# Performance work log

Hardware: AMD Instinct MI355X
Metric: run time of the kernel (lower is better)

Reference implementation:

```python
import jax, jax.numpy as jnp
import numpy as np


def setup_inputs() -> dict:
    key = jax.random.key(0)
    ks = jax.random.split(key, 8)
    B, C, H, W = 32, 98, 128, 128
    F, D = 256, 128
    return {
        "hm": jax.random.normal(ks[0], (B, C, H, W), dtype=jnp.float32),
        "feat": jax.random.normal(ks[1], (B, F, H, W), dtype=jnp.float32),
        "W_embed": jax.random.normal(ks[2], (2 + 1 + F, D), dtype=jnp.float32) * 0.05,
        "b_embed": jax.random.normal(ks[3], (D,), dtype=jnp.float32) * 0.05,
        "A": jax.random.normal(ks[4], (C, C), dtype=jnp.float32) * 0.05,
        "W_gcn": jax.random.normal(ks[5], (D, D), dtype=jnp.float32) * 0.05,
        "W_out": jax.random.normal(ks[6], (D, 2), dtype=jnp.float32) * 0.05,
        "b_out": jax.random.normal(ks[7], (2,), dtype=jnp.float32) * 0.05,
    }


def reference(hm, feat, W_embed, b_embed, A, W_gcn, W_out, b_out):
    # hm: [B, C, H, W] per-landmark heatmaps; feat: [B, F, H, W] backbone features.
    B, C, H, W = hm.shape
    F = feat.shape[1]

    # decode_heatmap: per-(batch, landmark) argmax location over HxW (batched,
    # replacing the original per-sample Python loops).
    hm_flat = hm.reshape(B, C, H * W)
    idx = jnp.argmax(hm_flat, axis=-1)                      # [B, C] int
    ys = idx // W
    xs = idx % W

    # node confidences: hm[i, classIds, ys, xs] -> batched gather
    conf = jnp.take_along_axis(hm_flat, idx[:, :, None], axis=-1)[..., 0]  # [B, C]

    # pooling_feature: gather the F-dim feature vector at each landmark location
    feat_flat = feat.reshape(B, F, H * W)
    vis = jnp.take_along_axis(feat_flat, idx[:, None, :], axis=-1)  # [B, F, C]
    vis = jnp.transpose(vis, (0, 2, 1))                              # [B, C, F]

    # normalized positions: node_positions (x, y) / hm_size [h, w] (as in source)
    hm_size = jnp.array([H, W], dtype=hm.dtype)
    pos = jnp.stack([xs, ys], axis=-1).astype(hm.dtype) / hm_size    # [B, C, 2]

    # GCN over landmarks (batched instead of per-sample calls)
    node = jnp.concatenate([pos, conf[..., None], vis], axis=-1)     # [B, C, 2+1+F]
    h0 = jax.nn.relu(jnp.einsum("bcf,fd->bcd", node, W_embed) + b_embed)
    h1 = jax.nn.relu(jnp.einsum("ij,bjd,de->bie", A, h0, W_gcn))     # learned adjacency
    out = jnp.einsum("bcd,do->bco", h1, W_out) + b_out               # [B, C, 2]
    return hm, out
```

## Files before the change

kernel.cpp:

```cpp
#include <hip/hip_runtime.h>

#define HM_B 32
#define HM_C 98
#define HM_H 128
#define HM_W 128
#define HWSZ (HM_H * HM_W)
#define FDIM 256
#define DDIM 128
#define NODE_F (2 + 1 + FDIM)
#define NODE_P 260
#define BC (HM_B * HM_C)
#define HM_ELEMS ((size_t)BC * HWSZ)
#define LCHUNK 8
#define ICHUNK 7
#define NTHR 256
#define NWAVE (NTHR / 64)

typedef float f32x4 __attribute__((ext_vector_type(4)));

__global__ __launch_bounds__(NTHR) void k1_copy_argmax(
    const float* __restrict__ hm, float* __restrict__ out_hm,
    float* __restrict__ pconf, int* __restrict__ pidx) {
    const int row = blockIdx.x;
    const int tid = threadIdx.x;
    const f32x4* __restrict__ src = (const f32x4*)(hm + (size_t)row * HWSZ);
    f32x4* __restrict__ dst = (f32x4*)(out_hm + (size_t)row * HWSZ);

    float bv = -INFINITY;
    int bi = 0;
    f32x4 cur0 = src[0 * NTHR + tid];
    f32x4 cur1 = src[1 * NTHR + tid];
    f32x4 cur2 = src[2 * NTHR + tid];
    f32x4 cur3 = src[3 * NTHR + tid];
    #pragma unroll
    for (int g = 0; g < 4; ++g) {
        f32x4 nxt0, nxt1, nxt2, nxt3;
        if (g < 3) {
            nxt0 = src[((g + 1) * 4 + 0) * NTHR + tid];
            nxt1 = src[((g + 1) * 4 + 1) * NTHR + tid];
            nxt2 = src[((g + 1) * 4 + 2) * NTHR + tid];
            nxt3 = src[((g + 1) * 4 + 3) * NTHR + tid];
        }
        #pragma unroll
        for (int u = 0; u < 4; ++u) {
            const f32x4 v = (u == 0) ? cur0 : (u == 1) ? cur1 : (u == 2) ? cur2 : cur3;
            const int p = (g * 4 + u) * NTHR + tid;
            __builtin_nontemporal_store(v, dst + p);
            const float m4 = fmaxf(fmaxf(v[0], v[1]), fmaxf(v[2], v[3]));
            if (m4 > bv) {
                const int base = p * 4;
                if (v[0] > bv) { bv = v[0]; bi = base; }
                if (v[1] > bv) { bv = v[1]; bi = base + 1; }
                if (v[2] > bv) { bv = v[2]; bi = base + 2; }
                if (v[3] > bv) { bv = v[3]; bi = base + 3; }
            }
        }
        cur0 = nxt0; cur1 = nxt1; cur2 = nxt2; cur3 = nxt3;
    }

    #pragma unroll
    for (int s = 1; s < 64; s <<= 1) {
        const float ov = __shfl_xor(bv, s, 64);
        const int oi = __shfl_xor(bi, s, 64);
        if (ov > bv || (ov == bv && oi < bi)) { bv = ov; bi = oi; }
    }
    if ((tid & 63) == 0) {
        pconf[row * NWAVE + (tid >> 6)] = bv;
        pidx[row * NWAVE + (tid >> 6)] = bi;
    }
}

__global__ __launch_bounds__(NTHR) void k2_embed(
    const float* __restrict__ feat, const float* __restrict__ pconf,
    const int* __restrict__ pidx, const float* __restrict__ W_embed,
    const float* __restrict__ b_embed, float* __restrict__ h0_ws) {
    const int bc0 = blockIdx.x * LCHUNK;
    const int tid = threadIdx.x;
    __shared__ float node_s[LCHUNK][NODE_P];
    __shared__ int locs[LCHUNK];

    if (tid < LCHUNK) {
        const int row = bc0 + tid;
        float fv = pconf[row * NWAVE];
        int fi = pidx[row * NWAVE];
        #pragma unroll
        for (int w = 1; w < NWAVE; ++w) {
            const float ov = pconf[row * NWAVE + w];
            const int oi = pidx[row * NWAVE + w];
            if (ov > fv || (ov == fv && oi < fi)) { fv = ov; fi = oi; }
        }
        locs[tid] = fi;
        node_s[tid][0] = (float)(fi % HM_W) * (1.0f / (float)HM_H);
        node_s[tid][1] = (float)(fi / HM_W) * (1.0f / (float)HM_W);
        node_s[tid][2] = fv;
    }
    __syncthreads();

    float g[LCHUNK];
    #pragma unroll
    for (int l = 0; l < LCHUNK; ++l) {
        const int bb = (bc0 + l) / HM_C;
        g[l] = __builtin_nontemporal_load(
            feat + ((size_t)(bb * FDIM + tid)) * HWSZ + locs[l]);
    }
    #pragma unroll
    for (int l = 0; l < LCHUNK; ++l)
        node_s[l][3 + tid] = g[l];
    __syncthreads();

    const int d = tid & (DDIM - 1);
    const int lbase = (tid >> 7) * 4;
    const float bias = b_embed[d];
    float a0 = bias, a1 = bias, a2 = bias, a3 = bias;
    for (int f = 0; f < NODE_F; ++f) {
        const float w = W_embed[f * DDIM + d];
        a0 = fmaf(node_s[lbase + 0][f], w, a0);
        a1 = fmaf(node_s[lbase + 1][f], w, a1);
        a2 = fmaf(node_s[lbase + 2][f], w, a2);
        a3 = fmaf(node_s[lbase + 3][f], w, a3);
    }
    h0_ws[(size_t)(bc0 + lbase + 0) * DDIM + d] = fmaxf(a0, 0.f);
    h0_ws[(size_t)(bc0 + lbase + 1) * DDIM + d] = fmaxf(a1, 0.f);
    h0_ws[(size_t)(bc0 + lbase + 2) * DDIM + d] = fmaxf(a2, 0.f);
    h0_ws[(size_t)(bc0 + lbase + 3) * DDIM + d] = fmaxf(a3, 0.f);
}

__global__ __launch_bounds__(DDIM) void k3_gcn(
    const float* __restrict__ A, const float* __restrict__ h0_ws,
    const float* __restrict__ W_gcn, const float* __restrict__ W_out,
    const float* __restrict__ b_out, float* __restrict__ out2) {
    const int b = blockIdx.x / (HM_C / ICHUNK);
    const int i0 = (blockIdx.x % (HM_C / ICHUNK)) * ICHUNK;
    const int tid = threadIdx.x;

    __shared__ float arow[ICHUNK * HM_C];
    __shared__ float tmp_s[ICHUNK * DDIM];
    __shared__ float h1_s[ICHUNK * DDIM];

    for (int k = tid; k < ICHUNK * HM_C; k += DDIM)
        arow[k] = A[(i0 + k / HM_C) * HM_C + (k % HM_C)];
    __syncthreads();

    {
        float acc[ICHUNK];
        #pragma unroll
        for (int i = 0; i < ICHUNK; ++i) acc[i] = 0.f;
        for (int j = 0; j < HM_C; ++j) {
            const float v = h0_ws[((size_t)b * HM_C + j) * DDIM + tid];
            #pragma unroll
            for (int i = 0; i < ICHUNK; ++i)
                acc[i] = fmaf(arow[i * HM_C + j], v, acc[i]);
        }
        #pragma unroll
        for (int i = 0; i < ICHUNK; ++i) tmp_s[i * DDIM + tid] = acc[i];
    }
    __syncthreads();

    {
        float acc[ICHUNK];
        #pragma unroll
        for (int i = 0; i < ICHUNK; ++i) acc[i] = 0.f;
        for (int k = 0; k < DDIM; ++k) {
            const float w = W_gcn[k * DDIM + tid];
            #pragma unroll
            for (int i = 0; i < ICHUNK; ++i)
                acc[i] = fmaf(tmp_s[i * DDIM + k], w, acc[i]);
        }
        #pragma unroll
        for (int i = 0; i < ICHUNK; ++i) h1_s[i * DDIM + tid] = fmaxf(acc[i], 0.f);
    }
    __syncthreads();

    if (tid < ICHUNK * 2) {
        const int i = tid >> 1;
        const int o = tid & 1;
        float acc = b_out[o];
        for (int dd = 0; dd < DDIM; ++dd)
            acc = fmaf(h1_s[i * DDIM + dd], W_out[dd * 2 + o], acc);
        out2[((size_t)b * HM_C + i0 + i) * 2 + o] = acc;
    }
}

extern "C" void kernel_launch(void* const* d_in, const int* in_sizes, int n_in,
                              void* d_out, int out_size, void* d_ws, size_t ws_size,
                              hipStream_t stream) {
    const float* hm      = (const float*)d_in[0];
    const float* feat    = (const float*)d_in[1];
    const float* W_embed = (const float*)d_in[2];
    const float* b_embed = (const float*)d_in[3];
    const float* A       = (const float*)d_in[4];
    const float* W_gcn   = (const float*)d_in[5];
    const float* W_out   = (const float*)d_in[6];
    const float* b_out   = (const float*)d_in[7];

    float* out_hm = (float*)d_out;
    float* out2   = (float*)d_out + HM_ELEMS;

    char* ws = (char*)d_ws;
    float* pconf = (float*)ws;  ws += BC * NWAVE * sizeof(float);
    int*   pidx  = (int*)ws;    ws += BC * NWAVE * sizeof(int);
    float* h0_ws = (float*)ws;

    k1_copy_argmax<<<BC, NTHR, 0, stream>>>(hm, out_hm, pconf, pidx);
    k2_embed<<<BC / LCHUNK, NTHR, 0, stream>>>(feat, pconf, pidx,
                                               W_embed, b_embed, h0_ws);
    k3_gcn<<<HM_B * (HM_C / ICHUNK), DDIM, 0, stream>>>(A, h0_ws, W_gcn,
                                                        W_out, b_out, out2);
}
```

Before: 109.6 us.

## Split fused heatmap copy and argmax into separate kernels

Separates the heatmap passthrough copy from the per-row argmax reduction. The argmax kernel now loads all 16 vectors per thread up front, and a grid-stride kernel with a fixed block count does the nontemporal copy. This decouples the store traffic from the reduction, but the heatmap is now read from memory twice, adding a full extra pass over a large tensor.

```diff
diff --git a/kernel.cpp b/kernel.cpp
--- a/kernel.cpp
+++ b/kernel.cpp
@@ -15,47 +15,35 @@
 #define ICHUNK 7
 #define NTHR 256
 #define NWAVE (NTHR / 64)
+#define COPY_BLOCKS 2048
 
 typedef float f32x4 __attribute__((ext_vector_type(4)));
 
-__global__ __launch_bounds__(NTHR) void k1_copy_argmax(
-    const float* __restrict__ hm, float* __restrict__ out_hm,
-    float* __restrict__ pconf, int* __restrict__ pidx) {
+__global__ __launch_bounds__(NTHR) void k1a_argmax(
+    const float* __restrict__ hm, float* __restrict__ pconf,
+    int* __restrict__ pidx) {
     const int row = blockIdx.x;
     const int tid = threadIdx.x;
     const f32x4* __restrict__ src = (const f32x4*)(hm + (size_t)row * HWSZ);
-    f32x4* __restrict__ dst = (f32x4*)(out_hm + (size_t)row * HWSZ);
+
+    f32x4 v[16];
+    #pragma unroll
+    for (int t = 0; t < 16; ++t)
+        v[t] = src[t * NTHR + tid];
 
     float bv = -INFINITY;
     int bi = 0;
-    f32x4 cur0 = src[0 * NTHR + tid];
-    f32x4 cur1 = src[1 * NTHR + tid];
-    f32x4 cur2 = src[2 * NTHR + tid];
-    f32x4 cur3 = src[3 * NTHR + tid];
-    #pragma unroll
-    for (int g = 0; g < 4; ++g) {
-        f32x4 nxt0, nxt1, nxt2, nxt3;
-        if (g < 3) {
-            nxt0 = src[((g + 1) * 4 + 0) * NTHR + tid];
-            nxt1 = src[((g + 1) * 4 + 1) * NTHR + tid];
-            nxt2 = src[((g + 1) * 4 + 2) * NTHR + tid];
-            nxt3 = src[((g + 1) * 4 + 3) * NTHR + tid];
-        }
-        #pragma unroll
-        for (int u = 0; u < 4; ++u) {
-            const f32x4 v = (u == 0) ? cur0 : (u == 1) ? cur1 : (u == 2) ? cur2 : cur3;
-            const int p = (g * 4 + u) * NTHR + tid;
-            __builtin_nontemporal_store(v, dst + p);
-            const float m4 = fmaxf(fmaxf(v[0], v[1]), fmaxf(v[2], v[3]));
-            if (m4 > bv) {
-                const int base = p * 4;
-                if (v[0] > bv) { bv = v[0]; bi = base; }
-                if (v[1] > bv) { bv = v[1]; bi = base + 1; }
-                if (v[2] > bv) { bv = v[2]; bi = base + 2; }
-                if (v[3] > bv) { bv = v[3]; bi = base + 3; }
-            }
-        }
-        cur0 = nxt0; cur1 = nxt1; cur2 = nxt2; cur3 = nxt3;
+    #pragma unroll
+    for (int t = 0; t < 16; ++t) {
+        const f32x4 x = v[t];
+        const int base = (t * NTHR + tid) * 4;
+        const float m4 = fmaxf(fmaxf(x[0], x[1]), fmaxf(x[2], x[3]));
+        if (m4 > bv) {
+            if (x[0] > bv) { bv = x[0]; bi = base; }
+            if (x[1] > bv) { bv = x[1]; bi = base + 1; }
+            if (x[2] > bv) { bv = x[2]; bi = base + 2; }
+            if (x[3] > bv) { bv = x[3]; bi = base + 3; }
+        }
     }
 
     #pragma unroll
@@ -67,6 +55,17 @@
     if ((tid & 63) == 0) {
         pconf[row * NWAVE + (tid >> 6)] = bv;
         pidx[row * NWAVE + (tid >> 6)] = bi;
+    }
+}
+
+__global__ __launch_bounds__(NTHR) void k1b_copy(
+    const float* __restrict__ hm, float* __restrict__ out_hm) {
+    const size_t stride = (size_t)COPY_BLOCKS * NTHR;
+    const f32x4* __restrict__ src = (const f32x4*)hm;
+    f32x4* __restrict__ dst = (f32x4*)out_hm;
+    for (size_t p = (size_t)blockIdx.x * NTHR + threadIdx.x;
+         p < HM_ELEMS / 4; p += stride) {
+        __builtin_nontemporal_store(src[p], dst + p);
     }
 }
 
@@ -201,7 +200,8 @@
     int*   pidx  = (int*)ws;    ws += BC * NWAVE * sizeof(int);
     float* h0_ws = (float*)ws;
 
-    k1_copy_argmax<<<BC, NTHR, 0, stream>>>(hm, out_hm, pconf, pidx);
+    k1a_argmax<<<BC, NTHR, 0, stream>>>(hm, pconf, pidx);
+    k1b_copy<<<COPY_BLOCKS, NTHR, 0, stream>>>(hm, out_hm);
     k2_embed<<<BC / LCHUNK, NTHR, 0, stream>>>(feat, pconf, pidx,
                                                W_embed, b_embed, h0_ws);
     k3_gcn<<<HM_B * (HM_C / ICHUNK), DDIM, 0, stream>>>(A, h0_ws, W_gcn,
```

Result: slower. 139.5 us (+27.3%).
